# Performance work log

Measured on AMD Instinct MI355X. Metric: run time of the kernel, lower is better.

## Reference

```python
import jax, jax.numpy as jnp
import numpy as np
import math

HIDDEN = 8
HEADS = 2
HEAD_DIM = HIDDEN // HEADS  # 4
MAX_SEQ = 102
B, S = 4096, 102


def _rotary_cache(seq_len, head_dim):
    # Matches _create_rotary_embeddings: dim = head_dim//2, inv_freq over arange(0, dim, 2)
    pos = jnp.arange(seq_len, dtype=jnp.float32)
    dim = head_dim // 2
    inv_freq = 1.0 / (10000.0 ** (jnp.arange(0, dim, 2, dtype=jnp.float32) / dim))
    sinusoid = pos[:, None] * inv_freq[None, :]           # [seq, dim//2] -> [102, 1]
    return jnp.stack([jnp.sin(sinusoid), jnp.cos(sinusoid)], axis=0)  # [2, seq, 1]


def _apply_rotary(x, cos, sin):
    # x: [B, H, S, hd]; cos/sin: [2, S, 1] (faithful to the source's buggy unpack,
    # which broadcasts the stacked sin/cos pair across the H==2 head dim)
    x2 = jnp.stack([-x[..., 1::2], x[..., ::2]], axis=-1).reshape(x.shape)
    return x * cos + x2 * sin


def setup_inputs() -> dict:
    key = jax.random.key(0)
    kq, kk, kv, k1, k2, k3, k4 = jax.random.split(key, 7)
    scale = 1.0 / math.sqrt(HIDDEN)
    return {
        "query": jax.random.normal(kq, (B, S, HIDDEN), dtype=jnp.float32),
        "key": jax.random.normal(kk, (B, S, HIDDEN), dtype=jnp.float32),
        "value": jax.random.normal(kv, (B, S, HIDDEN), dtype=jnp.float32),
        "wq": jax.random.normal(k1, (HIDDEN, HIDDEN), dtype=jnp.float32) * scale,
        "wk": jax.random.normal(k2, (HIDDEN, HIDDEN), dtype=jnp.float32) * scale,
        "wv": jax.random.normal(k3, (HIDDEN, HIDDEN), dtype=jnp.float32) * scale,
        "wo": jax.random.normal(k4, (HIDDEN, HIDDEN), dtype=jnp.float32) * scale,
    }


def reference(query, key, value, wq, wk, wv, wo):
    b, sq, _ = query.shape
    sk = key.shape[1]
    # nn.Linear (no bias): y = x @ W^T
    q = query @ wq.T
    k = key @ wk.T
    v = value @ wv.T
    # b n (h d) -> b h n d
    def split_heads(t, s):
        return t.reshape(b, s, HEADS, HEAD_DIM).transpose(0, 2, 1, 3)
    q = split_heads(q, sq)
    k = split_heads(k, sk)
    v = split_heads(v, sk)
    cache = _rotary_cache(MAX_SEQ, HEAD_DIM)
    sin_t = cache[:, :sq]  # [2, sq, 1] (named 'sin' in source, holds stacked sin/cos)
    cos_t = cache[:, :sk]  # [2, sk, 1]
    q = _apply_rotary(q, cos_t, sin_t)
    k = _apply_rotary(k, cos_t, sin_t)
    scale = 1.0 / math.sqrt(HEAD_DIM)
    # chunk_size = min(sk, 1024) = sk -> single chunk == full softmax attention
    scores = jnp.einsum('bhqd,bhkd->bhqk', q, k) * scale  # [B, H, Sq, Sk]
    attn = jax.nn.softmax(scores, axis=-1)
    out = jnp.einsum('bhqk,bhkd->bhqd', attn, v)
    # b h n d -> b n (h d)
    out = out.transpose(0, 2, 1, 3).reshape(b, sq, HIDDEN)
    return out @ wo.T
```

## Files before the change

### kernel.cpp

```cpp
#include <hip/hip_runtime.h>

#define NB  4096
#define SS  102
#define SSP 104
#define HID 8
#define RS  0.72134752044448170368f

typedef float v2f __attribute__((ext_vector_type(2)));

#define DOT8(A, B, W, i) \
    ((A).x*(W)[(i)*8+0] + (A).y*(W)[(i)*8+1] + (A).z*(W)[(i)*8+2] + (A).w*(W)[(i)*8+3] + \
     (B).x*(W)[(i)*8+4] + (B).y*(W)[(i)*8+5] + (B).z*(W)[(i)*8+6] + (B).w*(W)[(i)*8+7])

__global__ __launch_bounds__(128) void mha_fused_kernel(
    const float* __restrict__ query, const float* __restrict__ key,
    const float* __restrict__ value, const float* __restrict__ wq,
    const float* __restrict__ wk, const float* __restrict__ wv,
    const float* __restrict__ wo, float* __restrict__ out)
{
    __shared__ float sQ[2 * SSP * 4];
    __shared__ float sK[2 * SS * 4];
    __shared__ float sV[2 * SS * 4];

    const int t = threadIdx.x;
    const int b = blockIdx.x;

    if (t < SS) {
        const size_t boff = (size_t)b * (SS * HID);
        const float4* q4 = (const float4*)(query + boff) + 2 * t;
        const float4* k4 = (const float4*)(key   + boff) + 2 * t;
        const float4* v4 = (const float4*)(value + boff) + 2 * t;
        const float4 qa = q4[0], qb = q4[1];
        const float4 ka = k4[0], kb = k4[1];
        const float4 va = v4[0], vb = v4[1];
        const float sn = sinf((float)t), cn = cosf((float)t);

#pragma unroll
        for (int h = 0; h < 2; ++h) {
            const float wrk = h ? cn : sn;
            const float wrq = wrk * RS;
            float y[4], z[4];
#pragma unroll
            for (int u = 0; u < 2; ++u) {
                const int i0 = h * 4 + 2 * u;
                const float x0 = DOT8(qa, qb, wq, i0), x1 = DOT8(qa, qb, wq, i0 + 1);
                y[2*u] = (x0 - x1) * wrq;  y[2*u+1] = (x1 + x0) * wrq;
                const float k0 = DOT8(ka, kb, wk, i0), k1 = DOT8(ka, kb, wk, i0 + 1);
                z[2*u] = (k0 - k1) * wrk;  z[2*u+1] = (k1 + k0) * wrk;
            }
            ((float4*)sQ)[h * SSP + t] = make_float4(y[0], y[1], y[2], y[3]);
            ((float4*)sK)[h * SS  + t] = make_float4(z[0], z[1], z[2], z[3]);
            const float f0 = DOT8(va, vb, wv, h*4+0), f1 = DOT8(va, vb, wv, h*4+1);
            const float f2 = DOT8(va, vb, wv, h*4+2), f3 = DOT8(va, vb, wv, h*4+3);
            ((float4*)sV)[h * SS + t] = make_float4(f0, f1, f2, f3);
        }
    } else if (t < SSP) {
        ((float4*)sQ)[t]       = make_float4(0.f, 0.f, 0.f, 0.f);
        ((float4*)sQ)[SSP + t] = make_float4(0.f, 0.f, 0.f, 0.f);
    }
    __syncthreads();

    const int wid = t >> 6, lane = t & 63;
    const int h = wid;
    const bool act = lane < 52;
    v2f q0, q1, q2, q3;
    if (act) {
        const float4* Q4 = (const float4*)sQ + h * SSP + 2 * lane;
        const float4 qa = Q4[0], qc = Q4[1];
        q0 = (v2f){qa.x, qc.x}; q1 = (v2f){qa.y, qc.y};
        q2 = (v2f){qa.z, qc.z}; q3 = (v2f){qa.w, qc.w};
    }
    __syncthreads();

    if (act) {
        v2f acc0 = {0.f,0.f}, acc1 = {0.f,0.f}, acc2 = {0.f,0.f}, acc3 = {0.f,0.f};
        v2f l = {0.f, 0.f};
        const float4* K4 = (const float4*)sK + h * SS;
        const float4* V4 = (const float4*)sV + h * SS;
        float4 kk = K4[0], vvv = V4[0];
#pragma unroll 2
        for (int k = 1; k < SS; ++k) {
            const float4 nk = K4[k], nv = V4[k];
            v2f s = q0 * kk.x + q1 * kk.y + q2 * kk.z + q3 * kk.w;
            v2f p;
            p.x = __builtin_amdgcn_exp2f(s.x);
            p.y = __builtin_amdgcn_exp2f(s.y);
            l += p;
            acc0 += p * vvv.x; acc1 += p * vvv.y;
            acc2 += p * vvv.z; acc3 += p * vvv.w;
            kk = nk; vvv = nv;
        }
        {
            v2f s = q0 * kk.x + q1 * kk.y + q2 * kk.z + q3 * kk.w;
            v2f p;
            p.x = __builtin_amdgcn_exp2f(s.x);
            p.y = __builtin_amdgcn_exp2f(s.y);
            l += p;
            acc0 += p * vvv.x; acc1 += p * vvv.y;
            acc2 += p * vvv.z; acc3 += p * vvv.w;
        }
        const float ix = 1.f / l.x, iy = 1.f / l.y;
        float4* comb = (float4*)sQ;
        comb[4 * lane + h]     = make_float4(acc0.x*ix, acc1.x*ix, acc2.x*ix, acc3.x*ix);
        comb[4 * lane + 2 + h] = make_float4(acc0.y*iy, acc1.y*iy, acc2.y*iy, acc3.y*iy);
    }
    __syncthreads();

    if (t < SS) {
        const float4 c0 = ((const float4*)sQ)[2 * t];
        const float4 c1 = ((const float4*)sQ)[2 * t + 1];
        float o[8];
#pragma unroll
        for (int i = 0; i < 8; ++i) {
            o[i] = c0.x*wo[i*8+0] + c0.y*wo[i*8+1] + c0.z*wo[i*8+2] + c0.w*wo[i*8+3]
                 + c1.x*wo[i*8+4] + c1.y*wo[i*8+5] + c1.z*wo[i*8+6] + c1.w*wo[i*8+7];
        }
        float4* o4 = (float4*)(out + (size_t)b * (SS * HID) + t * HID);
        o4[0] = make_float4(o[0], o[1], o[2], o[3]);
        o4[1] = make_float4(o[4], o[5], o[6], o[7]);
    }
}

extern "C" void kernel_launch(void* const* d_in, const int* in_sizes, int n_in,
                              void* d_out, int out_size, void* d_ws, size_t ws_size,
                              hipStream_t stream) {
    const float* query = (const float*)d_in[0];
    const float* key   = (const float*)d_in[1];
    const float* value = (const float*)d_in[2];
    const float* wq    = (const float*)d_in[3];
    const float* wk    = (const float*)d_in[4];
    const float* wv    = (const float*)d_in[5];
    const float* wo    = (const float*)d_in[6];
    float* out = (float*)d_out;
    mha_fused_kernel<<<NB, 128, 0, stream>>>(query, key, value, wq, wk, wv, wo, out);
}
```

Baseline: 122.5 us.

## Split keys across waves and process four queries per lane

Each wave now handles half of the key range for both heads, and each lane handles four query rows instead of two, so every K/V shared-memory load feeds twice as many score computations. The two waves' partial sums and normalizers are combined through shared memory with an extra barrier before the output projection. This cuts LDS read traffic per flop but adds a merge step, more registers and a synchronization.

```diff
diff --git a/kernel.cpp b/kernel.cpp
--- a/kernel.cpp
+++ b/kernel.cpp
@@ -21,6 +21,7 @@
     __shared__ float sQ[2 * SSP * 4];
     __shared__ float sK[2 * SS * 4];
     __shared__ float sV[2 * SS * 4];
+    __shared__ float sL[2 * SSP];
 
     const int t = threadIdx.x;
     const int b = blockIdx.x;
@@ -61,54 +62,89 @@
     __syncthreads();
 
     const int wid = t >> 6, lane = t & 63;
-    const int h = wid;
+    const int kh = wid;
     const bool act = lane < 52;
-    v2f q0, q1, q2, q3;
+    const int h = (lane >= 26) ? 1 : 0;
+    const int g = lane - 26 * h;
+    const int r0 = 4 * g;
+
+    v2f q[2][4];
     if (act) {
-        const float4* Q4 = (const float4*)sQ + h * SSP + 2 * lane;
-        const float4 qa = Q4[0], qc = Q4[1];
-        q0 = (v2f){qa.x, qc.x}; q1 = (v2f){qa.y, qc.y};
-        q2 = (v2f){qa.z, qc.z}; q3 = (v2f){qa.w, qc.w};
+        const float4* Q4 = (const float4*)sQ + h * SSP + r0;
+        const float4 f0 = Q4[0], f1 = Q4[1], f2 = Q4[2], f3 = Q4[3];
+        q[0][0] = (v2f){f0.x, f1.x}; q[0][1] = (v2f){f0.y, f1.y};
+        q[0][2] = (v2f){f0.z, f1.z}; q[0][3] = (v2f){f0.w, f1.w};
+        q[1][0] = (v2f){f2.x, f3.x}; q[1][1] = (v2f){f2.y, f3.y};
+        q[1][2] = (v2f){f2.z, f3.z}; q[1][3] = (v2f){f2.w, f3.w};
     }
     __syncthreads();
 
+    v2f acc[2][4], l[2];
+#pragma unroll
+    for (int P = 0; P < 2; ++P) {
+        l[P] = (v2f){0.f, 0.f};
+#pragma unroll
+        for (int d = 0; d < 4; ++d) acc[P][d] = (v2f){0.f, 0.f};
+    }
     if (act) {
-        v2f acc0 = {0.f,0.f}, acc1 = {0.f,0.f}, acc2 = {0.f,0.f}, acc3 = {0.f,0.f};
-        v2f l = {0.f, 0.f};
-        const float4* K4 = (const float4*)sK + h * SS;
-        const float4* V4 = (const float4*)sV + h * SS;
-        float4 kk = K4[0], vvv = V4[0];
+        const float4* K4 = (const float4*)sK + h * SS + 51 * kh;
+        const float4* V4 = (const float4*)sV + h * SS + 51 * kh;
+        float4 kk = K4[0], vv = V4[0];
 #pragma unroll 2
-        for (int k = 1; k < SS; ++k) {
-            const float4 nk = K4[k], nv = V4[k];
-            v2f s = q0 * kk.x + q1 * kk.y + q2 * kk.z + q3 * kk.w;
-            v2f p;
-            p.x = __builtin_amdgcn_exp2f(s.x);
-            p.y = __builtin_amdgcn_exp2f(s.y);
-            l += p;
-            acc0 += p * vvv.x; acc1 += p * vvv.y;
-            acc2 += p * vvv.z; acc3 += p * vvv.w;
-            kk = nk; vvv = nv;
+        for (int j = 1; j < 51; ++j) {
+            const float4 nk = K4[j], nv = V4[j];
+#pragma unroll
+            for (int P = 0; P < 2; ++P) {
+                v2f s = q[P][0]*kk.x + q[P][1]*kk.y + q[P][2]*kk.z + q[P][3]*kk.w;
+                v2f p; p.x = __builtin_amdgcn_exp2f(s.x); p.y = __builtin_amdgcn_exp2f(s.y);
+                l[P] += p;
+                acc[P][0] += p*vv.x; acc[P][1] += p*vv.y;
+                acc[P][2] += p*vv.z; acc[P][3] += p*vv.w;
+            }
+            kk = nk; vv = nv;
         }
-        {
-            v2f s = q0 * kk.x + q1 * kk.y + q2 * kk.z + q3 * kk.w;
-            v2f p;
-            p.x = __builtin_amdgcn_exp2f(s.x);
-            p.y = __builtin_amdgcn_exp2f(s.y);
-            l += p;
-            acc0 += p * vvv.x; acc1 += p * vvv.y;
-            acc2 += p * vvv.z; acc3 += p * vvv.w;
+#pragma unroll
+        for (int P = 0; P < 2; ++P) {
+            v2f s = q[P][0]*kk.x + q[P][1]*kk.y + q[P][2]*kk.z + q[P][3]*kk.w;
+            v2f p; p.x = __builtin_amdgcn_exp2f(s.x); p.y = __builtin_amdgcn_exp2f(s.y);
+            l[P] += p;
+            acc[P][0] += p*vv.x; acc[P][1] += p*vv.y;
+            acc[P][2] += p*vv.z; acc[P][3] += p*vv.w;
         }
-        const float ix = 1.f / l.x, iy = 1.f / l.y;
-        float4* comb = (float4*)sQ;
-        comb[4 * lane + h]     = make_float4(acc0.x*ix, acc1.x*ix, acc2.x*ix, acc3.x*ix);
-        comb[4 * lane + 2 + h] = make_float4(acc0.y*iy, acc1.y*iy, acc2.y*iy, acc3.y*iy);
+    }
+
+    if (act && kh == 1) {
+        float4* A = (float4*)sQ + h * SSP + r0;
+        A[0] = make_float4(acc[0][0].x, acc[0][1].x, acc[0][2].x, acc[0][3].x);
+        A[1] = make_float4(acc[0][0].y, acc[0][1].y, acc[0][2].y, acc[0][3].y);
+        A[2] = make_float4(acc[1][0].x, acc[1][1].x, acc[1][2].x, acc[1][3].x);
+        A[3] = make_float4(acc[1][0].y, acc[1][1].y, acc[1][2].y, acc[1][3].y);
+        ((float4*)sL)[h * 26 + g] = make_float4(l[0].x, l[0].y, l[1].x, l[1].y);
+    }
+    __syncthreads();
+
+    if (act && kh == 0) {
+        float4* A = (float4*)sQ + h * SSP + r0;
+        const float4 pa0 = A[0], pa1 = A[1], pa2 = A[2], pa3 = A[3];
+        const float4 pl  = ((const float4*)sL)[h * 26 + g];
+        const float i0 = 1.f / (l[0].x + pl.x);
+        const float i1 = 1.f / (l[0].y + pl.y);
+        const float i2 = 1.f / (l[1].x + pl.z);
+        const float i3 = 1.f / (l[1].y + pl.w);
+        A[0] = make_float4((acc[0][0].x+pa0.x)*i0, (acc[0][1].x+pa0.y)*i0,
+                           (acc[0][2].x+pa0.z)*i0, (acc[0][3].x+pa0.w)*i0);
+        A[1] = make_float4((acc[0][0].y+pa1.x)*i1, (acc[0][1].y+pa1.y)*i1,
+                           (acc[0][2].y+pa1.z)*i1, (acc[0][3].y+pa1.w)*i1);
+        A[2] = make_float4((acc[1][0].x+pa2.x)*i2, (acc[1][1].x+pa2.y)*i2,
+                           (acc[1][2].x+pa2.z)*i2, (acc[1][3].x+pa2.w)*i2);
+        A[3] = make_float4((acc[1][0].y+pa3.x)*i3, (acc[1][1].y+pa3.y)*i3,
+                           (acc[1][2].y+pa3.z)*i3, (acc[1][3].y+pa3.w)*i3);
     }
     __syncthreads();
 
     if (t < SS) {
-        const float4 c0 = ((const float4*)sQ)[2 * t];
-        const float4 c1 = ((const float4*)sQ)[2 * t + 1];
+        const float4 c0 = ((const float4*)sQ)[t];
+        const float4 c1 = ((const float4*)sQ)[SSP + t];
         float o[8];
 #pragma unroll
         for (int i = 0; i < 8; ++i) {
```

Result: faster. 119.7 us (-2.3%).
